# Kernel optimization log

Hardware: AMD Instinct MI355X
Metric: run time of the kernel (lower is better)

## Reference

```python
import jax, jax.numpy as jnp
import numpy as np

N_PAPER, N_MESH = 60000, 30000
N = N_PAPER + N_MESH
E_TRAIN, E_DEC = 2000000, 400000
F_PAPER = F_MESH = 128
D0, H, D = 16, 32, 16  # initial embed, hidden, final embed
NREL, NB = 2, 4


def _glorot(key, shape):
    fan_in, fan_out = shape[-2], shape[-1]
    s = jnp.sqrt(6.0 / (fan_in + fan_out)).astype(jnp.float32)
    return jax.random.uniform(key, shape, jnp.float32, -s, s)


def setup_inputs() -> dict:
    key = jax.random.key(0)
    ks = iter(jax.random.split(key, 40))
    inp = {
        'x_paper': jax.random.normal(next(ks), (N_PAPER, F_PAPER), jnp.float32),
        'x_mesh': jax.random.normal(next(ks), (N_MESH, F_MESH), jnp.float32),
        'train_edge_index': jax.random.randint(next(ks), (2, E_TRAIN), 0, N, jnp.int64 if jax.config.jax_enable_x64 else jnp.int32),
        'train_edge_type': jnp.sort(jax.random.randint(next(ks), (E_TRAIN,), 0, NREL)),
        'pos_edge_index': jax.random.randint(next(ks), (2, E_DEC), 0, N),
        'pos_edge_type': jnp.sort(jax.random.randint(next(ks), (E_DEC,), 0, NREL)),
        'neg_edge_index': jax.random.randint(next(ks), (2, E_DEC), 0, N),
        'neg_edge_type': jnp.sort(jax.random.randint(next(ks), (E_DEC,), 0, NREL)),
        # input transforms
        'Wp': _glorot(next(ks), (F_PAPER, D0)), 'bp': jnp.zeros((D0,), jnp.float32),
        'Wm': _glorot(next(ks), (F_MESH, D0)), 'bm': jnp.zeros((D0,), jnp.float32),
        # decode linears
        'Wd0': _glorot(next(ks), (D, D)), 'bd0': jnp.zeros((D,), jnp.float32),
        'Wd1': _glorot(next(ks), (D, D)), 'bd1': jnp.zeros((D,), jnp.float32),
    }
    dims = [(D0, H), (H, H), (H, H), (H, D)]
    for i, (di, do) in enumerate(dims, 1):
        inp[f'bases{i}'] = _glorot(next(ks), (NB, di, do))
        inp[f'comp{i}'] = _glorot(next(ks), (NREL, NB))
        inp[f'root{i}'] = _glorot(next(ks), (di, do))
        inp[f'bias{i}'] = jnp.zeros((do,), jnp.float32)
    return inp


def rgcn_layer(x, src, dst, et, bases, comp, root, bias):
    # PyG RGCNConv with basis decomposition, per-relation mean aggregation.
    out = x @ root + bias
    xs = x[src]  # [E, in]
    for r in range(NREL):
        W_r = jnp.einsum('b,bio->io', comp[r], bases)
        m = xs @ W_r  # [E, out]
        mf = (et == r).astype(m.dtype)
        cnt = jax.ops.segment_sum(mf, dst, num_segments=N)
        agg = jax.ops.segment_sum(m * mf[:, None], dst, num_segments=N)
        out = out + agg / jnp.clip(cnt, 1.0)[:, None]
    return out


def _decode_block(z, ei, et, Wd0, bd0, Wd1, bd1):
    zs, zd = z[ei[0]], z[ei[1]]
    h0 = zs @ Wd0 + bd0
    h1 = zs @ Wd1 + bd1
    h = jnp.where((et == 0)[:, None], h0, h1)
    return jnp.sum(h * zd, axis=-1)


def reference(x_paper, x_mesh, train_edge_index, train_edge_type,
              pos_edge_index, pos_edge_type, neg_edge_index, neg_edge_type,
              Wp, bp, Wm, bm, Wd0, bd0, Wd1, bd1,
              bases1, comp1, root1, bias1, bases2, comp2, root2, bias2,
              bases3, comp3, root3, bias3, bases4, comp4, root4, bias4):
    x = jnp.concatenate([x_paper @ Wp + bp, x_mesh @ Wm + bm], axis=0)  # [N, D0]
    src, dst = train_edge_index[0], train_edge_index[1]
    x = jax.nn.relu(rgcn_layer(x, src, dst, train_edge_type, bases1, comp1, root1, bias1))
    x = jax.nn.relu(rgcn_layer(x, src, dst, train_edge_type, bases2, comp2, root2, bias2))
    x = jax.nn.relu(rgcn_layer(x, src, dst, train_edge_type, bases3, comp3, root3, bias3))
    z = rgcn_layer(x, src, dst, train_edge_type, bases4, comp4, root4, bias4)
    # edge types are sorted, so per-edge in-order compute matches the masked concat order
    pos = _decode_block(z, pos_edge_index, pos_edge_type, Wd0, bd0, Wd1, bd1)
    neg = _decode_block(z, neg_edge_index, neg_edge_type, Wd0, bd0, Wd1, bd1)
    return jnp.concatenate([pos, neg], axis=0)  # [2*E_DEC]
```

## Files before the change

### kernel.cpp

```cpp
#include <hip/hip_runtime.h>
#include <hip/hip_bf16.h>

constexpr int NN = 90000;
constexpr int NP = 60000;
constexpr int NM = 30000;
constexpr int ET = 2000000;
constexpr int ED = 400000;
constexpr int TWO_NN = 2 * NN;

constexpr int BKT_SH  = 9;
constexpr int NB_BKT  = (TWO_NN + 511) >> BKT_SH;
constexpr int BKT_CAP = 6400;
constexpr int TILE    = 2048;
constexpr int N_TILES = (ET + TILE - 1) / TILE;

__device__ __forceinline__ float bflo(unsigned int u) {
    union { unsigned int i; float f; } c;
    c.i = u << 16;
    return c.f;
}
__device__ __forceinline__ float bfhi(unsigned int u) {
    union { unsigned int i; float f; } c;
    c.i = u & 0xffff0000u;
    return c.f;
}
__device__ __forceinline__ unsigned short f2bf(float f) {
    union { float f; unsigned int i; } c;
    c.f = f;
    unsigned int x = c.i;
    return (unsigned short)((x + 0x7FFFu + ((x >> 16) & 1u)) >> 16);
}

__global__ void init_kernel(const int* __restrict__ tei, int* __restrict__ gcur,
                            int* __restrict__ dflag) {
    int b = blockIdx.x * blockDim.x + threadIdx.x;
    if (b < NB_BKT) gcur[b] = b * BKT_CAP;
    if (b == 0) {
        int allzero = 1;
        for (int i = 0; i < 16; i++)
            if (tei[2 * i + 1] != 0) allzero = 0;
        dflag[0] = allzero;
    }
}

__global__ void __launch_bounds__(256) binA_kernel(
        const int* __restrict__ ei, const int* __restrict__ et,
        const int* __restrict__ dflag, int* __restrict__ gcur,
        int2* __restrict__ pairs) {
    __shared__ int histw[4][NB_BKT];
    __shared__ int wbase[4][NB_BKT];
    __shared__ int tot[NB_BKT];
    __shared__ int excl[NB_BKT];
    __shared__ int gbase[NB_BKT];
    __shared__ int scn[256];
    __shared__ int2 tbuf[TILE];
    int t = threadIdx.x;
    int w = t >> 6;
    int tile0 = blockIdx.x * TILE;
    int tcount = ET - tile0;
    if (tcount > TILE) tcount = TILE;
    for (int i = t; i < 4 * NB_BKT; i += 256) ((int*)histw)[i] = 0;
    __syncthreads();
    int sft = dflag[0];
    int myk[8], mys[8];
#pragma unroll
    for (int q = 0; q < 8; q++) {
        int li = q * 256 + t;
        myk[q] = -1;
        if (li < tcount) {
            int e = tile0 + li;
            int s = ei[(size_t)e << sft];
            int d = ei[(size_t)(ET + e) << sft];
            int r = et[(size_t)e << sft];
            int key = r * NN + d;
            myk[q] = key;
            mys[q] = s;
            atomicAdd(&histw[w][key >> BKT_SH], 1);
        }
    }
    __syncthreads();
    for (int i = t; i < NB_BKT; i += 256) {
        int h0 = histw[0][i], h1 = histw[1][i], h2 = histw[2][i], h3 = histw[3][i];
        wbase[0][i] = 0;
        wbase[1][i] = h0;
        wbase[2][i] = h0 + h1;
        wbase[3][i] = h0 + h1 + h2;
        tot[i] = h0 + h1 + h2 + h3;
    }
    __syncthreads();
    int v0 = (t < NB_BKT / 2) ? tot[2 * t] : 0;
    int v1 = (t < NB_BKT / 2) ? tot[2 * t + 1] : 0;
    int s = v0 + v1;
    scn[t] = s;
    __syncthreads();
    for (int st = 1; st < 256; st <<= 1) {
        int u = (t >= st) ? scn[t - st] : 0;
        __syncthreads();
        scn[t] += u;
        __syncthreads();
    }
    int base = scn[t] - s;
    if (t < NB_BKT / 2) {
        excl[2 * t] = base;
        excl[2 * t + 1] = base + v0;
    }
    __syncthreads();
    for (int i = t; i < NB_BKT; i += 256) {
        int e0 = excl[i];
        wbase[0][i] += e0;
        wbase[1][i] += e0;
        wbase[2][i] += e0;
        wbase[3][i] += e0;
        histw[0][i] = 0; histw[1][i] = 0; histw[2][i] = 0; histw[3][i] = 0;
    }
    __syncthreads();
#pragma unroll
    for (int q = 0; q < 8; q++) {
        if (myk[q] >= 0) {
            int b = myk[q] >> BKT_SH;
            int p = wbase[w][b] + atomicAdd(&histw[w][b], 1);
            tbuf[p] = make_int2(myk[q], mys[q]);
        }
    }
    __syncthreads();
    for (int i = t; i < NB_BKT; i += 256)
        if (tot[i] > 0) gbase[i] = atomicAdd(&gcur[i], tot[i]);
    __syncthreads();
    for (int i = t; i < tcount; i += 256) {
        int2 p = tbuf[i];
        int b = p.x >> BKT_SH;
        int gpos = gbase[b] + (i - excl[b]);
        int cap = (b + 1) * BKT_CAP - 1;
        pairs[gpos < cap ? gpos : cap] = p;
    }
}

__global__ void __launch_bounds__(256) histplace_kernel(
        const int* __restrict__ gcur, const int2* __restrict__ pairs,
        int* __restrict__ off, int* __restrict__ endo, float* __restrict__ inv,
        int* __restrict__ csr) {
    __shared__ int kh[512];
    __shared__ int scn[256];
    int b = blockIdx.x;
    int t = threadIdx.x;
    int beg = b * BKT_CAP, end = gcur[b];
    for (int i = t; i < 512; i += 256) kh[i] = 0;
    __syncthreads();
    for (int i = beg + t; i < end; i += 256)
        atomicAdd(&kh[pairs[i].x & 511], 1);
    __syncthreads();
    int v[2];
    int s = 0;
#pragma unroll
    for (int q = 0; q < 2; q++) {
        v[q] = kh[t * 2 + q];
        s += v[q];
    }
    scn[t] = s;
    __syncthreads();
    for (int st = 1; st < 256; st <<= 1) {
        int u = (t >= st) ? scn[t - st] : 0;
        __syncthreads();
        scn[t] += u;
        __syncthreads();
    }
    int run = beg + scn[t] - s;
    int kbase = b << BKT_SH;
    int kc[2];
#pragma unroll
    for (int q = 0; q < 2; q++) {
        int key = kbase + t * 2 + q;
        if (key < TWO_NN) {
            off[key] = run;
            endo[key] = run + v[q];
            inv[key] = 1.0f / (float)(v[q] > 1 ? v[q] : 1);
        }
        kc[q] = run;
        run += v[q];
    }
    __syncthreads();
#pragma unroll
    for (int q = 0; q < 2; q++) kh[t * 2 + q] = kc[q];
    __syncthreads();
    for (int i = beg + t; i < end; i += 256) {
        int2 p = pairs[i];
        int pos = atomicAdd(&kh[p.x & 511], 1);
        csr[pos] = p.y;
    }
}

__global__ void __launch_bounds__(256) embed2_kernel(
        const float* __restrict__ Xp, const float* __restrict__ Xm,
        const float* __restrict__ Wp, const float* __restrict__ bp,
        const float* __restrict__ Wm, const float* __restrict__ bm,
        unsigned short* __restrict__ outbf) {
    __shared__ float Wl[4096 + 32];
    for (int i = threadIdx.x; i < 2048; i += 256) {
        Wl[i] = Wp[i];
        Wl[2048 + i] = Wm[i];
    }
    if (threadIdx.x < 16) {
        Wl[4096 + threadIdx.x] = bp[threadIdx.x];
        Wl[4112 + threadIdx.x] = bm[threadIdx.x];
    }
    __syncthreads();
    int n = blockIdx.x * 256 + threadIdx.x;
    if (n >= NN) return;
    const float* X;
    const float* Ws;
    const float* Bs;
    if (n < NP) { X = Xp + (size_t)n * 128; Ws = Wl; Bs = Wl + 4096; }
    else        { X = Xm + (size_t)(n - NP) * 128; Ws = Wl + 2048; Bs = Wl + 4112; }
    float acc[16];
#pragma unroll
    for (int j = 0; j < 16; j++) acc[j] = Bs[j];
    const float4* row = (const float4*)X;
    for (int k4 = 0; k4 < 32; k4++) {
        float4 xv = row[k4];
        int k = k4 * 4;
#pragma unroll
        for (int j = 0; j < 16; j++) {
            float a = acc[j];
            a = fmaf(xv.x, Ws[(k + 0) * 16 + j], a);
            a = fmaf(xv.y, Ws[(k + 1) * 16 + j], a);
            a = fmaf(xv.z, Ws[(k + 2) * 16 + j], a);
            a = fmaf(xv.w, Ws[(k + 3) * 16 + j], a);
            acc[j] = a;
        }
    }
    ushort4* ob = (ushort4*)(outbf + (size_t)n * 16);
#pragma unroll
    for (int q = 0; q < 4; q++) {
        ushort4 ub;
        ub.x = f2bf(acc[4 * q]);     ub.y = f2bf(acc[4 * q + 1]);
        ub.z = f2bf(acc[4 * q + 2]); ub.w = f2bf(acc[4 * q + 3]);
        ob[q] = ub;
    }
}

__global__ void prep_all_kernel(
        const float* __restrict__ ba0, const float* __restrict__ co0,
        const float* __restrict__ ro0, const float* __restrict__ bi0,
        const float* __restrict__ ba1, const float* __restrict__ co1,
        const float* __restrict__ ro1, const float* __restrict__ bi1,
        const float* __restrict__ ba2, const float* __restrict__ co2,
        const float* __restrict__ ro2, const float* __restrict__ bi2,
        const float* __restrict__ ba3, const float* __restrict__ co3,
        const float* __restrict__ ro3, const float* __restrict__ bi3,
        float* __restrict__ Wbuf4) {
    int l = blockIdx.x;
    const float* bases; const float* comp; const float* root; const float* bias;
    if (l == 0)      { bases = ba0; comp = co0; root = ro0; bias = bi0; }
    else if (l == 1) { bases = ba1; comp = co1; root = ro1; bias = bi1; }
    else if (l == 2) { bases = ba2; comp = co2; root = ro2; bias = bi2; }
    else             { bases = ba3; comp = co3; root = ro3; bias = bi3; }
    int din = (l == 0) ? 16 : 32;
    int dout = (l == 3) ? 16 : 32;
    int sz = din * dout;
    float* W = Wbuf4 + l * 3200;
    for (int i = threadIdx.x; i < sz; i += 256) {
        float b0 = bases[i];
        float b1 = bases[sz + i];
        float b2 = bases[2 * sz + i];
        float b3 = bases[3 * sz + i];
        for (int r = 0; r < 2; r++) {
            W[r * sz + i] = comp[r * 4 + 0] * b0 + comp[r * 4 + 1] * b1 +
                            comp[r * 4 + 2] * b2 + comp[r * 4 + 3] * b3;
        }
        W[2 * sz + i] = root[i];
    }
    if (threadIdx.x < dout) W[3 * sz + threadIdx.x] = bias[threadIdx.x];
}

template <int DIN, int DOUT, int RELU>
__global__ void __launch_bounds__(256) layer_kernel(
        const int* __restrict__ off, const int* __restrict__ endo,
        const int* __restrict__ csr,
        const unsigned short* __restrict__ xbf_in,
        const float* __restrict__ inv, const float* __restrict__ Wbuf,
        unsigned short* __restrict__ xbf_out) {
    constexpr int SZ = DIN * DOUT;
    constexpr int QL = DIN / 8;
    constexpr int TPN = 2 * QL;
    constexpr int NPB = 256 / TPN;
    constexpr int AGST = 2 * DIN + 4;
    constexpr int XSST = DIN + 4;
    __shared__ float Wl[3 * SZ + DOUT];
    __shared__ float agg[NPB * AGST];
    __shared__ float xs[NPB * XSST];
    for (int i = threadIdx.x; i < 3 * SZ + DOUT; i += 256) Wl[i] = Wbuf[i];
    int t = threadIdx.x;
    int ln = t / TPN;
    int rl = t % TPN;
    int r = rl / QL;
    int lane = rl % QL;
    int d = blockIdx.x * NPB + ln;
    if (d < NN) {
        if (r == 0) {
            uint4 u = *(const uint4*)(xbf_in + (size_t)d * DIN + lane * 8);
            float* xp = xs + ln * XSST + lane * 8;
            xp[0] = bflo(u.x); xp[1] = bfhi(u.x);
            xp[2] = bflo(u.y); xp[3] = bfhi(u.y);
            xp[4] = bflo(u.z); xp[5] = bfhi(u.z);
            xp[6] = bflo(u.w); xp[7] = bfhi(u.w);
        }
        int key = r * NN + d;
        int b = off[key];
        int e = endo[key];
        float a0[8] = {0, 0, 0, 0, 0, 0, 0, 0};
        float a1[8] = {0, 0, 0, 0, 0, 0, 0, 0};
        const unsigned short* hp = xbf_in + lane * 8;
        int k = b;
        for (; k + 1 < e; k += 2) {
            int s0 = csr[k];
            int s1 = csr[k + 1];
            uint4 u0 = *(const uint4*)(hp + (size_t)s0 * DIN);
            uint4 u1 = *(const uint4*)(hp + (size_t)s1 * DIN);
            a0[0] += bflo(u0.x); a0[1] += bfhi(u0.x);
            a0[2] += bflo(u0.y); a0[3] += bfhi(u0.y);
            a0[4] += bflo(u0.z); a0[5] += bfhi(u0.z);
            a0[6] += bflo(u0.w); a0[7] += bfhi(u0.w);
            a1[0] += bflo(u1.x); a1[1] += bfhi(u1.x);
            a1[2] += bflo(u1.y); a1[3] += bfhi(u1.y);
            a1[4] += bflo(u1.z); a1[5] += bfhi(u1.z);
            a1[6] += bflo(u1.w); a1[7] += bfhi(u1.w);
        }
        if (k < e) {
            uint4 u0 = *(const uint4*)(hp + (size_t)csr[k] * DIN);
            a0[0] += bflo(u0.x); a0[1] += bfhi(u0.x);
            a0[2] += bflo(u0.y); a0[3] += bfhi(u0.y);
            a0[4] += bflo(u0.z); a0[5] += bfhi(u0.z);
            a0[6] += bflo(u0.w); a0[7] += bfhi(u0.w);
        }
        float* ap = agg + ln * AGST + r * DIN + lane * 8;
        *(float4*)ap = make_float4(a0[0] + a1[0], a0[1] + a1[1],
                                   a0[2] + a1[2], a0[3] + a1[3]);
        *(float4*)(ap + 4) = make_float4(a0[4] + a1[4], a0[5] + a1[5],
                                         a0[6] + a1[6], a0[7] + a1[7]);
    }
    __syncthreads();
    constexpr int CPN = DOUT / 4;
    for (int tt = t; tt < NPB * CPN; tt += 256) {
        int ln2 = tt / CPN;
        int j0 = (tt % CPN) * 4;
        int d2 = blockIdx.x * NPB + ln2;
        if (d2 < NN) {
            float iv0 = inv[d2], iv1 = inv[NN + d2];
            float acc[4];
#pragma unroll
            for (int jj = 0; jj < 4; jj++) acc[jj] = Wl[3 * SZ + j0 + jj];
#pragma unroll
            for (int k = 0; k < DIN; k++) {
                float xv = xs[ln2 * XSST + k];
                float m0 = agg[ln2 * AGST + k] * iv0;
                float m1 = agg[ln2 * AGST + DIN + k] * iv1;
                const float* w0 = &Wl[k * DOUT + j0];
                const float* w1 = &Wl[SZ + k * DOUT + j0];
                const float* wr = &Wl[2 * SZ + k * DOUT + j0];
#pragma unroll
                for (int jj = 0; jj < 4; jj++) {
                    acc[jj] = fmaf(xv, wr[jj], acc[jj]);
                    acc[jj] = fmaf(m0, w0[jj], acc[jj]);
                    acc[jj] = fmaf(m1, w1[jj], acc[jj]);
                }
            }
            if (RELU) {
#pragma unroll
                for (int jj = 0; jj < 4; jj++) acc[jj] = fmaxf(acc[jj], 0.0f);
            }
            ushort4 ub;
            ub.x = f2bf(acc[0]); ub.y = f2bf(acc[1]);
            ub.z = f2bf(acc[2]); ub.w = f2bf(acc[3]);
            *(ushort4*)(xbf_out + (size_t)d2 * DOUT + j0) = ub;
        }
    }
}

__global__ void __launch_bounds__(256) decode_fused_kernel(
        const unsigned short* __restrict__ zbf,
        const float* __restrict__ Wd0, const float* __restrict__ bd0,
        const float* __restrict__ Wd1, const float* __restrict__ bd1,
        const int* __restrict__ pei, const int* __restrict__ pet,
        const int* __restrict__ nei, const int* __restrict__ net_,
        float* __restrict__ out, const int* __restrict__ dflag) {
    __shared__ float W[2][256];
    __shared__ float B[2][16];
    for (int i = threadIdx.x; i < 256; i += 256) {
        W[0][i] = Wd0[i];
        W[1][i] = Wd1[i];
    }
    if (threadIdx.x < 16) {
        B[0][threadIdx.x] = bd0[threadIdx.x];
        B[1][threadIdx.x] = bd1[threadIdx.x];
    }
    __syncthreads();
    int i = blockIdx.x * 256 + threadIdx.x;
    if (i >= 2 * ED) return;
    int sft = dflag[0];
    const int* ei;
    const int* et;
    int e;
    if (i < ED) { ei = pei; et = pet; e = i; }
    else        { ei = nei; et = net_; e = i - ED; }
    int s = ei[(size_t)e << sft];
    int d = ei[(size_t)(ED + e) << sft];
    int r = et[(size_t)e << sft];
    float zs[16], zd[16];
    const uint4* sp = (const uint4*)(zbf + ((size_t)s << 4));
    const uint4* dp = (const uint4*)(zbf + ((size_t)d << 4));
#pragma unroll
    for (int h = 0; h < 2; h++) {
        uint4 us = sp[h];
        uint4 ud = dp[h];
        int o8 = h * 8;
        zs[o8 + 0] = bflo(us.x); zs[o8 + 1] = bfhi(us.x);
        zs[o8 + 2] = bflo(us.y); zs[o8 + 3] = bfhi(us.y);
        zs[o8 + 4] = bflo(us.z); zs[o8 + 5] = bfhi(us.z);
        zs[o8 + 6] = bflo(us.w); zs[o8 + 7] = bfhi(us.w);
        zd[o8 + 0] = bflo(ud.x); zd[o8 + 1] = bfhi(ud.x);
        zd[o8 + 2] = bflo(ud.y); zd[o8 + 3] = bfhi(ud.y);
        zd[o8 + 4] = bflo(ud.z); zd[o8 + 5] = bfhi(ud.z);
        zd[o8 + 6] = bflo(ud.w); zd[o8 + 7] = bfhi(ud.w);
    }
    const float* Wr = W[r];
    const float* Br = B[r];
    float acc = 0.0f;
#pragma unroll
    for (int j = 0; j < 16; j++) {
        float yj = Br[j];
#pragma unroll
        for (int k = 0; k < 16; k++) yj = fmaf(zs[k], Wr[k * 16 + j], yj);
        acc = fmaf(yj, zd[j], acc);
    }
    out[i] = acc;
}

extern "C" void kernel_launch(void* const* d_in, const int* in_sizes, int n_in,
                              void* d_out, int out_size, void* d_ws, size_t ws_size,
                              hipStream_t stream) {
    const float* x_paper = (const float*)d_in[0];
    const float* x_mesh  = (const float*)d_in[1];
    const int* tei  = (const int*)d_in[2];
    const int* tet  = (const int*)d_in[3];
    const int* pei  = (const int*)d_in[4];
    const int* pet  = (const int*)d_in[5];
    const int* nei  = (const int*)d_in[6];
    const int* net_ = (const int*)d_in[7];
    const float* Wp  = (const float*)d_in[8];
    const float* bp  = (const float*)d_in[9];
    const float* Wm  = (const float*)d_in[10];
    const float* bm  = (const float*)d_in[11];
    const float* Wd0 = (const float*)d_in[12];
    const float* bd0 = (const float*)d_in[13];
    const float* Wd1 = (const float*)d_in[14];
    const float* bd1 = (const float*)d_in[15];

    float* ws = (float*)d_ws;
    size_t o = 0;
    unsigned short* xbfA = (unsigned short*)(ws + o); o += (size_t)NN * 16;
    unsigned short* xbfB = (unsigned short*)(ws + o); o += (size_t)NN * 16;
    float* inv  = ws + o; o += (size_t)TWO_NN;
    int*   off  = (int*)(ws + o); o += (size_t)TWO_NN;
    int*   endo = (int*)(ws + o); o += (size_t)TWO_NN;
    int*   csr  = (int*)(ws + o); o += (size_t)NB_BKT * BKT_CAP;
    int*   gcur = (int*)(ws + o); o += 512;
    int2*  pairs = (int2*)(ws + o); o += (size_t)2 * NB_BKT * BKT_CAP;
    float* Wbuf4 = ws + o; o += 4 * 3200;
    int*   dflag = (int*)(ws + o); o += 16;

    init_kernel<<<(NB_BKT + 255) / 256, 256, 0, stream>>>(tei, gcur, dflag);

    binA_kernel<<<N_TILES, 256, 0, stream>>>(tei, tet, dflag, gcur, pairs);
    histplace_kernel<<<NB_BKT, 256, 0, stream>>>(gcur, pairs, off, endo, inv, csr);

    embed2_kernel<<<(NN + 255) / 256, 256, 0, stream>>>(
        x_paper, x_mesh, Wp, bp, Wm, bm, xbfA);

    prep_all_kernel<<<4, 256, 0, stream>>>(
        (const float*)d_in[16], (const float*)d_in[17], (const float*)d_in[18], (const float*)d_in[19],
        (const float*)d_in[20], (const float*)d_in[21], (const float*)d_in[22], (const float*)d_in[23],
        (const float*)d_in[24], (const float*)d_in[25], (const float*)d_in[26], (const float*)d_in[27],
        (const float*)d_in[28], (const float*)d_in[29], (const float*)d_in[30], (const float*)d_in[31],
        Wbuf4);

    int blk16 = (NN + 63) / 64;
    int blk32 = (NN + 31) / 32;
    layer_kernel<16, 32, 1><<<blk16, 256, 0, stream>>>(
        off, endo, csr, xbfA, inv, Wbuf4 + 0 * 3200, xbfB);
    layer_kernel<32, 32, 1><<<blk32, 256, 0, stream>>>(
        off, endo, csr, xbfB, inv, Wbuf4 + 1 * 3200, xbfA);
    layer_kernel<32, 32, 1><<<blk32, 256, 0, stream>>>(
        off, endo, csr, xbfA, inv, Wbuf4 + 2 * 3200, xbfB);
    layer_kernel<32, 16, 0><<<blk32, 256, 0, stream>>>(
        off, endo, csr, xbfB, inv, Wbuf4 + 3 * 3200, xbfA);

    decode_fused_kernel<<<(2 * ED + 255) / 256, 256, 0, stream>>>(
        xbfA, Wd0, bd0, Wd1, bd1, pei, pet, nei, net_, (float*)d_out, dflag);
}
```

Measured before the change: 372.1 us.

## Tune RGCN layer kernel: larger blocks, bf16 smem, nontemporal CSR loads/stores

Raises the layer kernel block size from 256 to 512 threads with an occupancy hint in launch bounds. Self features are kept in shared memory as raw bf16 and unpacked two at a time inside the matmul loop. CSR index loads and output stores become nontemporal to reduce cache pollution, and the inner loop is unrolled by two over the input dimension. The nontemporal output store may hurt the next layer, which reads that output back through the gather.

```diff
diff --git a/kernel.cpp b/kernel.cpp
--- a/kernel.cpp
+++ b/kernel.cpp
@@ -272,8 +272,8 @@
     if (threadIdx.x < dout) W[3 * sz + threadIdx.x] = bias[threadIdx.x];
 }
 
-template <int DIN, int DOUT, int RELU>
-__global__ void __launch_bounds__(256) layer_kernel(
+template <int DIN, int DOUT, int RELU, int BS>
+__global__ void __launch_bounds__(BS, 8) layer_kernel(
         const int* __restrict__ off, const int* __restrict__ endo,
         const int* __restrict__ csr,
         const unsigned short* __restrict__ xbf_in,
@@ -282,13 +282,13 @@
     constexpr int SZ = DIN * DOUT;
     constexpr int QL = DIN / 8;
     constexpr int TPN = 2 * QL;
-    constexpr int NPB = 256 / TPN;
+    constexpr int NPB = BS / TPN;
     constexpr int AGST = 2 * DIN + 4;
-    constexpr int XSST = DIN + 4;
+    constexpr int XSST = DIN + 8;
     __shared__ float Wl[3 * SZ + DOUT];
     __shared__ float agg[NPB * AGST];
-    __shared__ float xs[NPB * XSST];
-    for (int i = threadIdx.x; i < 3 * SZ + DOUT; i += 256) Wl[i] = Wbuf[i];
+    __shared__ unsigned short xsu[NPB * XSST];
+    for (int i = threadIdx.x; i < 3 * SZ + DOUT; i += BS) Wl[i] = Wbuf[i];
     int t = threadIdx.x;
     int ln = t / TPN;
     int rl = t % TPN;
@@ -298,11 +298,7 @@
     if (d < NN) {
         if (r == 0) {
             uint4 u = *(const uint4*)(xbf_in + (size_t)d * DIN + lane * 8);
-            float* xp = xs + ln * XSST + lane * 8;
-            xp[0] = bflo(u.x); xp[1] = bfhi(u.x);
-            xp[2] = bflo(u.y); xp[3] = bfhi(u.y);
-            xp[4] = bflo(u.z); xp[5] = bfhi(u.z);
-            xp[6] = bflo(u.w); xp[7] = bfhi(u.w);
+            *(uint4*)&xsu[ln * XSST + lane * 8] = u;
         }
         int key = r * NN + d;
         int b = off[key];
@@ -312,8 +308,8 @@
         const unsigned short* hp = xbf_in + lane * 8;
         int k = b;
         for (; k + 1 < e; k += 2) {
-            int s0 = csr[k];
-            int s1 = csr[k + 1];
+            int s0 = __builtin_nontemporal_load(csr + k);
+            int s1 = __builtin_nontemporal_load(csr + k + 1);
             uint4 u0 = *(const uint4*)(hp + (size_t)s0 * DIN);
             uint4 u1 = *(const uint4*)(hp + (size_t)s1 * DIN);
             a0[0] += bflo(u0.x); a0[1] += bfhi(u0.x);
@@ -326,7 +322,8 @@
             a1[6] += bflo(u1.w); a1[7] += bfhi(u1.w);
         }
         if (k < e) {
-            uint4 u0 = *(const uint4*)(hp + (size_t)csr[k] * DIN);
+            int s0 = __builtin_nontemporal_load(csr + k);
+            uint4 u0 = *(const uint4*)(hp + (size_t)s0 * DIN);
             a0[0] += bflo(u0.x); a0[1] += bfhi(u0.x);
             a0[2] += bflo(u0.y); a0[3] += bfhi(u0.y);
             a0[4] += bflo(u0.z); a0[5] += bfhi(u0.z);
@@ -340,7 +337,7 @@
     }
     __syncthreads();
     constexpr int CPN = DOUT / 4;
-    for (int tt = t; tt < NPB * CPN; tt += 256) {
+    for (int tt = t; tt < NPB * CPN; tt += BS) {
         int ln2 = tt / CPN;
         int j0 = (tt % CPN) * 4;
         int d2 = blockIdx.x * NPB + ln2;
@@ -350,18 +347,25 @@
 #pragma unroll
             for (int jj = 0; jj < 4; jj++) acc[jj] = Wl[3 * SZ + j0 + jj];
 #pragma unroll
-            for (int k = 0; k < DIN; k++) {
-                float xv = xs[ln2 * XSST + k];
-                float m0 = agg[ln2 * AGST + k] * iv0;
-                float m1 = agg[ln2 * AGST + DIN + k] * iv1;
-                const float* w0 = &Wl[k * DOUT + j0];
-                const float* w1 = &Wl[SZ + k * DOUT + j0];
-                const float* wr = &Wl[2 * SZ + k * DOUT + j0];
+            for (int k2 = 0; k2 < DIN; k2 += 2) {
+                unsigned up = *(const unsigned*)&xsu[ln2 * XSST + k2];
+                float xv0 = bflo(up);
+                float xv1 = bfhi(up);
+                float m00 = agg[ln2 * AGST + k2] * iv0;
+                float m10 = agg[ln2 * AGST + DIN + k2] * iv1;
+                float m01 = agg[ln2 * AGST + k2 + 1] * iv0;
+                float m11 = agg[ln2 * AGST + DIN + k2 + 1] * iv1;
+                const float* w0a = &Wl[k2 * DOUT + j0];
+                const float* w1a = &Wl[SZ + k2 * DOUT + j0];
+                const float* wra = &Wl[2 * SZ + k2 * DOUT + j0];
 #pragma unroll
                 for (int jj = 0; jj < 4; jj++) {
-                    acc[jj] = fmaf(xv, wr[jj], acc[jj]);
-                    acc[jj] = fmaf(m0, w0[jj], acc[jj]);
-                    acc[jj] = fmaf(m1, w1[jj], acc[jj]);
+                    acc[jj] = fmaf(xv0, wra[jj], acc[jj]);
+                    acc[jj] = fmaf(m00, w0a[jj], acc[jj]);
+                    acc[jj] = fmaf(m10, w1a[jj], acc[jj]);
+                    acc[jj] = fmaf(xv1, wra[DOUT + jj], acc[jj]);
+                    acc[jj] = fmaf(m01, w0a[DOUT + jj], acc[jj]);
+                    acc[jj] = fmaf(m11, w1a[DOUT + jj], acc[jj]);
                 }
             }
             if (RELU) {
@@ -371,7 +375,10 @@
             ushort4 ub;
             ub.x = f2bf(acc[0]); ub.y = f2bf(acc[1]);
             ub.z = f2bf(acc[2]); ub.w = f2bf(acc[3]);
-            *(ushort4*)(xbf_out + (size_t)d2 * DOUT + j0) = ub;
+            union { ushort4 v; unsigned long long q; } pk;
+            pk.v = ub;
+            __builtin_nontemporal_store(
+                pk.q, (unsigned long long*)(xbf_out + (size_t)d2 * DOUT + j0));
         }
     }
 }
@@ -483,15 +490,16 @@
         (const float*)d_in[28], (const float*)d_in[29], (const float*)d_in[30], (const float*)d_in[31],
         Wbuf4);
 
-    int blk16 = (NN + 63) / 64;
-    int blk32 = (NN + 31) / 32;
-    layer_kernel<16, 32, 1><<<blk16, 256, 0, stream>>>(
+    constexpr int LBS = 512;
+    int blk16 = (NN + 127) / 128;
+    int blk32 = (NN + 63) / 64;
+    layer_kernel<16, 32, 1, LBS><<<blk16, LBS, 0, stream>>>(
         off, endo, csr, xbfA, inv, Wbuf4 + 0 * 3200, xbfB);
-    layer_kernel<32, 32, 1><<<blk32, 256, 0, stream>>>(
+    layer_kernel<32, 32, 1, LBS><<<blk32, LBS, 0, stream>>>(
         off, endo, csr, xbfB, inv, Wbuf4 + 1 * 3200, xbfA);
-    layer_kernel<32, 32, 1><<<blk32, 256, 0, stream>>>(
+    layer_kernel<32, 32, 1, LBS><<<blk32, LBS, 0, stream>>>(
         off, endo, csr, xbfA, inv, Wbuf4 + 2 * 3200, xbfB);
-    layer_kernel<32, 16, 0><<<blk32, 256, 0, stream>>>(
+    layer_kernel<32, 16, 0, LBS><<<blk32, LBS, 0, stream>>>(
         off, endo, csr, xbfB, inv, Wbuf4 + 3 * 3200, xbfA);
 
     decode_fused_kernel<<<(2 * ED + 255) / 256, 256, 0, stream>>>(
```

Measured after the change: 399.2 us. 7.3% more time.
